# Performance work log

Measured on AMD Instinct MI355X. Metric: run time of the kernel, lower is better.

The kernel has to match this reference:

```python
import jax, jax.numpy as jnp
import numpy as np

E = 30000          # nEdges
K_PER_EDGE = 12    # quadruplets per edge
KMAX = 16          # padded K dimension
Q = E * K_PER_EDGE # nQuadruplets = 360000
I = 180000         # intermediate (db) expansion size
DE, DQ, DB = 128, 64, 64   # emb_size_edge, emb_size_quad, emb_size_bilinear
DRBF, DCBF, DSBF = 16, 16, 32
NSPH = 32
SCALE_SILU = 1.0 / 0.6


def _act(x):
    # GemNet ScaledSiLU
    return jax.nn.silu(x) * SCALE_SILU


def setup_inputs() -> dict:
    key = jax.random.key(0)
    ks = jax.random.split(key, 16)
    inp = {}
    inp["m"] = jax.random.normal(ks[0], (E, DE), jnp.float32)
    inp["rbf"] = jax.random.normal(ks[1], (E, DRBF), jnp.float32)
    inp["cbf"] = jax.random.normal(ks[2], (I, DCBF), jnp.float32)
    inp["sbf_W1"] = jax.random.normal(ks[3], (E, DSBF, NSPH), jnp.float32) * 0.1
    inp["sph"] = jax.random.normal(ks[4], (E, KMAX, NSPH), jnp.float32) * 0.1
    # structured, valid scatter indices: 12 distinct K-slots per edge
    inp["Kidx4"] = jnp.tile(jnp.arange(K_PER_EDGE, dtype=jnp.int32), E)
    inp["id4_reduce_ca"] = jnp.repeat(jnp.arange(E, dtype=jnp.int32), K_PER_EDGE)
    inp["id_swap"] = jax.random.permutation(ks[5], E).astype(jnp.int32)
    inp["id4_expand_intm_db"] = jax.random.randint(ks[6], (I,), 0, E, jnp.int32)
    inp["id4_expand_abd"] = jax.random.randint(ks[7], (Q,), 0, I, jnp.int32)
    # parameters (bias-free Dense layers + bilinear weight + scaling factors)
    def w(k, shape, fan_in):
        return jax.random.normal(k, shape, jnp.float32) / np.sqrt(fan_in)
    inp["W_db"] = w(ks[8], (DE, DE), DE)
    inp["W_rbf"] = w(ks[9], (DRBF, DE), DRBF)
    inp["W_down"] = w(ks[10], (DE, DQ), DE)
    inp["W_cbf"] = w(ks[11], (DCBF, DQ), DCBF)
    inp["W_bilin"] = w(ks[12], (DQ, DSBF, DB), DQ * DSBF)
    inp["W_up_ca"] = w(ks[13], (DB, DE), DB)
    inp["W_up_ac"] = w(ks[14], (DB, DE), DB)
    inp["s_rbf"] = jnp.asarray(1.1, jnp.float32)
    inp["s_cbf"] = jnp.asarray(0.9, jnp.float32)
    inp["s_sbf"] = jnp.asarray(1.2, jnp.float32)
    return inp


def reference(m, rbf, cbf, sbf_W1, sph,
              W_db, W_rbf, W_down, W_cbf, W_bilin, W_up_ca, W_up_ac,
              s_rbf, s_cbf, s_sbf,
              Kidx4, id_swap, id4_reduce_ca, id4_expand_intm_db, id4_expand_abd):
    # dense_db + hadamard with rbf MLP + scale
    x_db = _act(m @ W_db)                        # (E, DE)
    x_db = (x_db * (rbf @ W_rbf)) * s_rbf        # scale_rbf scales the product
    # down projection to quad size, expand to intermediate set
    x_db = _act(x_db @ W_down)                   # (E, DQ)
    x_db = x_db[id4_expand_intm_db]              # (I, DQ)
    # hadamard with cbf MLP + scale, expand to quadruplets
    x_db = (x_db * (cbf @ W_cbf)) * s_cbf        # (I, DQ)
    x_db = x_db[id4_expand_abd]                  # (Q, DQ)
    # EfficientInteractionBilinear: scatter quads into padded (E, Kmax, DQ)
    m2 = jnp.zeros((E, KMAX, DQ), x_db.dtype).at[id4_reduce_ca, Kidx4].set(x_db)
    sum_k = jnp.einsum("eks,ekq->esq", sph, m2)          # (E, NSPH, DQ)
    rw = jnp.einsum("eis,esq->eiq", sbf_W1, sum_k)       # (E, DSBF, DQ)
    x = jnp.einsum("eiq,qib->eb", rw, W_bilin)           # (E, DB)
    x = x * s_sbf                                         # scale_sbf_sum
    # up projections; swap directions for ac
    x_ca = _act(x @ W_up_ca)                     # (E, DE)
    x_ac = _act(x @ W_up_ac)[id_swap]            # (E, DE)
    return (x_ca + x_ac) * (1.0 / np.sqrt(2.0))
```

## Files before the change

kernel.cpp:

```cpp
#include <hip/hip_runtime.h>
#include <hip/hip_bf16.h>


#define E_N   30000
#define KPE   12
#define KMAXX 16
#define I_N   180000
#define DE    128
#define DQ    64
#define DB    64
#define DRBF  16
#define DCBF  16
#define DSBF  32
#define NSPH  32
#define SCALE_SILU (1.0f/0.6f)
#define INV_SQRT2  0.70710678118654752f

typedef __attribute__((ext_vector_type(8))) short bf16x8;
typedef __attribute__((ext_vector_type(4))) float f32x4;

__device__ __forceinline__ float silu_scaled(float x) {
    return x / (1.0f + __expf(-x)) * SCALE_SILU;
}

__device__ __forceinline__ short f2bf(float x) {
    unsigned u = __float_as_uint(x);
    u += 0x7fffu + ((u >> 16) & 1u);
    return (short)(u >> 16);
}

__device__ __forceinline__ bf16x8 cvt8(const float4 a, const float4 b) {
    bf16x8 t;
    t[0]=f2bf(a.x); t[1]=f2bf(a.y); t[2]=f2bf(a.z); t[3]=f2bf(a.w);
    t[4]=f2bf(b.x); t[5]=f2bf(b.y); t[6]=f2bf(b.z); t[7]=f2bf(b.w);
    return t;
}

#define PK_WDBT   0
#define PK_WRBFT  16384
#define PK_WDOWNT 20480
#define PK_WUPAT  28672
#define PK_WUPBT  36864
#define PK_BT     45056
#define PK_TOTAL  176128

__global__ __launch_bounds__(256) void kw_prep(
    const float* __restrict__ Wdb, const float* __restrict__ Wrbf,
    const float* __restrict__ Wdown, const float* __restrict__ WupA,
    const float* __restrict__ WupB, const float* __restrict__ Wbil,
    ushort* __restrict__ wpk)
{
    const int idx = blockIdx.x * 256 + threadIdx.x;
    float v;
    if (idx < PK_WRBFT) {
        const int n = idx >> 7, k = idx & 127;
        v = Wdb[k * DE + n];
    } else if (idx < PK_WDOWNT) {
        const int j = idx - PK_WRBFT;
        const int n = j >> 5, k = j & 31;
        v = (k < DRBF) ? Wrbf[k * DE + n] : 0.f;
    } else if (idx < PK_WUPAT) {
        const int j = idx - PK_WDOWNT;
        const int q = j >> 7, k = j & 127;
        v = Wdown[k * DQ + q];
    } else if (idx < PK_WUPBT) {
        const int j = idx - PK_WUPAT;
        const int d = j >> 6, b = j & 63;
        v = WupA[b * DE + d];
    } else if (idx < PK_BT) {
        const int j = idx - PK_WUPBT;
        const int d = j >> 6, b = j & 63;
        v = WupB[b * DE + d];
    } else {
        const int j = idx - PK_BT;
        const int b = j >> 11, jj = j & 2047;
        const int i = jj >> 6, q = jj & 63;
        v = Wbil[(size_t)(q * DSBF + i) * DB + b];
    }
    wpk[idx] = (ushort)f2bf(v);
}

__global__ __launch_bounds__(256) void k1_mfma(
    const float* __restrict__ m, const float* __restrict__ rbf,
    const ushort* __restrict__ wpk, const float* __restrict__ s_rbf_p,
    ushort* __restrict__ Tb)
{
    const int l  = threadIdx.x & 63;
    const int wv = __builtin_amdgcn_readfirstlane(threadIdx.x >> 6);
    const int e0 = (blockIdx.x * 4 + wv) * 16;
    if (e0 >= E_N) return;
    const int mr = l & 15;
    const int kg = l >> 4;
    const ushort* WdbT  = wpk + PK_WDBT;
    const ushort* WrbfT = wpk + PK_WRBFT;

    f32x4 accH[8], accR[8];
    #pragma unroll
    for (int nt = 0; nt < 8; ++nt)
        #pragma unroll
        for (int r = 0; r < 4; ++r) { accH[nt][r] = 0.f; accR[nt][r] = 0.f; }

    bf16x8 ra;
    if (kg < 2) {
        const float* rr = rbf + (size_t)(e0 + mr) * DRBF + kg * 8;
        ra = cvt8(*(const float4*)rr, *(const float4*)(rr + 4));
    } else {
        #pragma unroll
        for (int j = 0; j < 8; ++j) ra[j] = 0;
    }
    #pragma unroll
    for (int nt = 0; nt < 8; ++nt) {
        const bf16x8 rb = *(const bf16x8*)(WrbfT + (nt*16 + mr)*32 + kg*8);
        accR[nt] = __builtin_amdgcn_mfma_f32_16x16x32_bf16(ra, rb, accR[nt], 0,0,0);
    }

    const float* mrow = m + (size_t)(e0 + mr) * DE + kg * 8;
    #pragma unroll
    for (int kt = 0; kt < 4; ++kt) {
        const float* ms = mrow + kt * 32;
        const bf16x8 a = cvt8(*(const float4*)ms, *(const float4*)(ms + 4));
        #pragma unroll
        for (int nt = 0; nt < 8; ++nt) {
            const bf16x8 b = *(const bf16x8*)(WdbT + (nt*16 + mr)*128 + kt*32 + kg*8);
            accH[nt] = __builtin_amdgcn_mfma_f32_16x16x32_bf16(a, b, accH[nt], 0,0,0);
        }
    }

    const float srbf = s_rbf_p[0];
    ushort* tout = Tb + (size_t)(e0 + kg*4) * DE + mr;
    #pragma unroll
    for (int nt = 0; nt < 8; ++nt)
        #pragma unroll
        for (int r = 0; r < 4; ++r)
            tout[(size_t)r * DE + 16*nt] =
                (ushort)f2bf(silu_scaled(accH[nt][r]) * accR[nt][r] * srbf);
}

__global__ __launch_bounds__(256) void k1b_mfma(
    const ushort* __restrict__ Tb, const ushort* __restrict__ wpk,
    float* __restrict__ xq)
{
    const int l  = threadIdx.x & 63;
    const int wv = __builtin_amdgcn_readfirstlane(threadIdx.x >> 6);
    const int e0 = (blockIdx.x * 4 + wv) * 16;
    if (e0 >= E_N) return;
    const int mr = l & 15;
    const int kg = l >> 4;
    const ushort* WdownT = wpk + PK_WDOWNT;

    f32x4 acc[4];
    #pragma unroll
    for (int nt = 0; nt < 4; ++nt)
        #pragma unroll
        for (int r = 0; r < 4; ++r) acc[nt][r] = 0.f;

    const ushort* arow = Tb + (size_t)(e0 + mr) * DE + kg * 8;
    #pragma unroll
    for (int kt = 0; kt < 4; ++kt) {
        const bf16x8 a = *(const bf16x8*)(arow + kt * 32);
        #pragma unroll
        for (int nt = 0; nt < 4; ++nt) {
            const bf16x8 b = *(const bf16x8*)(WdownT + (nt*16 + mr)*128 + kt*32 + kg*8);
            acc[nt] = __builtin_amdgcn_mfma_f32_16x16x32_bf16(a, b, acc[nt], 0,0,0);
        }
    }
    float* xout = xq + (size_t)(e0 + kg*4) * DQ + mr;
    #pragma unroll
    for (int nt = 0; nt < 4; ++nt)
        #pragma unroll
        for (int r = 0; r < 4; ++r)
            xout[(size_t)r * DQ + 16*nt] = silu_scaled(acc[nt][r]);
}

__global__ __launch_bounds__(256) void k2_intm(
    const float* __restrict__ cbf, const int* __restrict__ idx_db,
    const float* __restrict__ xq, const float* __restrict__ Wcbf,
    const float* __restrict__ s_cbf_p, float* __restrict__ y)
{
    __shared__ float sW[DCBF*DQ];
    for (int i = threadIdx.x; i < DCBF*DQ; i += 256) sW[i] = Wcbf[i];
    __syncthreads();
    const float sc = s_cbf_p[0];
    const int lane = threadIdx.x & 63;
    const int wv = __builtin_amdgcn_readfirstlane(threadIdx.x >> 6);
    for (int row = blockIdx.x*4 + wv; row < I_N; row += gridDim.x*4) {
        const float* cr = cbf + (size_t)row*DCBF;
        float acc = 0.f;
        #pragma unroll
        for (int k = 0; k < DCBF; ++k) acc += cr[k] * sW[k*DQ + lane];
        const int src = idx_db[row];
        y[(size_t)row*DQ + lane] = xq[(size_t)src*DQ + lane] * acc * sc;
    }
}

__global__ __launch_bounds__(256) void k3a_rw(
    const float* __restrict__ y, const float* __restrict__ sph,
    const float* __restrict__ sbf, const int* __restrict__ kidx,
    const int* __restrict__ abd, ushort* __restrict__ rw)
{
    const int l  = threadIdx.x & 63;
    const int wv = __builtin_amdgcn_readfirstlane(threadIdx.x >> 6);
    const int e  = blockIdx.x*4 + wv;
    const int q0 = l & 15;
    const int sg = l >> 4;
    const int s0 = sg * 8;

    float SK[8][4];
    #pragma unroll
    for (int r = 0; r < 8; ++r)
        #pragma unroll
        for (int c = 0; c < 4; ++c) SK[r][c] = 0.f;

    const int base = e * KPE;
    #pragma unroll
    for (int j = 0; j < KPE; ++j) {
        const int kj = kidx[base + j];
        const int aj = abd[base + j];
        const float* yr = y + (size_t)aj * DQ;
        const float v0 = yr[q0];
        const float v1 = yr[q0 + 16];
        const float v2 = yr[q0 + 32];
        const float v3 = yr[q0 + 48];
        const float* sp = sph + ((size_t)e * KMAXX + kj) * NSPH + s0;
        const float4 sA = *(const float4*)sp;
        const float4 sB = *(const float4*)(sp + 4);
        const float sv[8] = {sA.x, sA.y, sA.z, sA.w, sB.x, sB.y, sB.z, sB.w};
        #pragma unroll
        for (int r = 0; r < 8; ++r) {
            SK[r][0] = __builtin_fmaf(sv[r], v0, SK[r][0]);
            SK[r][1] = __builtin_fmaf(sv[r], v1, SK[r][1]);
            SK[r][2] = __builtin_fmaf(sv[r], v2, SK[r][2]);
            SK[r][3] = __builtin_fmaf(sv[r], v3, SK[r][3]);
        }
    }

    bf16x8 bfrag[4];
    #pragma unroll
    for (int qt = 0; qt < 4; ++qt) {
        bf16x8 t;
        #pragma unroll
        for (int r = 0; r < 8; ++r) t[r] = f2bf(SK[r][qt]);
        bfrag[qt] = t;
    }

    const float* sb0 = sbf + ((size_t)e * DSBF + q0) * NSPH + s0;
    bf16x8 afrag[2];
    #pragma unroll
    for (int h = 0; h < 2; ++h) {
        const float* ar = sb0 + h * 16 * NSPH;
        afrag[h] = cvt8(*(const float4*)ar, *(const float4*)(ar + 4));
    }

    f32x4 acc[2][4];
    #pragma unroll
    for (int h = 0; h < 2; ++h)
        #pragma unroll
        for (int qt = 0; qt < 4; ++qt)
            #pragma unroll
            for (int r = 0; r < 4; ++r) acc[h][qt][r] = 0.f;

    #pragma unroll
    for (int h = 0; h < 2; ++h)
        #pragma unroll
        for (int qt = 0; qt < 4; ++qt)
            acc[h][qt] = __builtin_amdgcn_mfma_f32_16x16x32_bf16(
                afrag[h], bfrag[qt], acc[h][qt], 0, 0, 0);

    ushort* ro = rw + (size_t)e * (DSBF * DQ);
    #pragma unroll
    for (int h = 0; h < 2; ++h)
        #pragma unroll
        for (int r = 0; r < 4; ++r) {
            const int i = h * 16 + sg * 4 + r;
            #pragma unroll
            for (int qt = 0; qt < 4; ++qt)
                ro[i * DQ + q0 + 16 * qt] = (ushort)f2bf(acc[h][qt][r]);
        }
}

__global__ __launch_bounds__(256) void k3b_bilin(
    const ushort* __restrict__ rw, const ushort* __restrict__ wpk,
    const float* __restrict__ s_sbf_p, ushort* __restrict__ Xb)
{
    const int l  = threadIdx.x & 63;
    const int wv = __builtin_amdgcn_readfirstlane(threadIdx.x >> 6);
    const int e0 = (blockIdx.x * 4 + wv) * 16;
    if (e0 >= E_N) return;
    const int m  = l & 15;
    const int kg = l >> 4;
    const ushort* BT = wpk + PK_BT;

    const ushort* arow = rw + (size_t)(e0 + m) * 2048 + kg * 8;
    const ushort* b0   = BT + (size_t)m * 2048 + kg * 8;

    f32x4 acc[4];
    #pragma unroll
    for (int qt = 0; qt < 4; ++qt)
        #pragma unroll
        for (int r = 0; r < 4; ++r) acc[qt][r] = 0.f;

    #pragma unroll 4
    for (int kt = 0; kt < 64; ++kt) {
        const bf16x8 a = *(const bf16x8*)(arow + kt * 32);
        #pragma unroll
        for (int qt = 0; qt < 4; ++qt) {
            const bf16x8 b = *(const bf16x8*)(b0 + (size_t)qt * 16 * 2048 + kt * 32);
            acc[qt] = __builtin_amdgcn_mfma_f32_16x16x32_bf16(a, b, acc[qt], 0, 0, 0);
        }
    }

    const float ss = s_sbf_p[0];
    ushort* xout = Xb + (size_t)(e0 + kg*4) * DQ + m;
    #pragma unroll
    for (int qt = 0; qt < 4; ++qt)
        #pragma unroll
        for (int r = 0; r < 4; ++r)
            xout[(size_t)r * DQ + 16*qt] = (ushort)f2bf(acc[qt][r] * ss);
}

__global__ __launch_bounds__(256) void k4_mfma(
    const ushort* __restrict__ Xb, const ushort* __restrict__ wpk,
    float* __restrict__ Ab, float* __restrict__ Bb)
{
    const int l  = threadIdx.x & 63;
    const int wv = __builtin_amdgcn_readfirstlane(threadIdx.x >> 6);
    const int e0 = (blockIdx.x * 4 + wv) * 16;
    if (e0 >= E_N) return;
    const int mr = l & 15;
    const int kg = l >> 4;
    const ushort* WupAT = wpk + PK_WUPAT;
    const ushort* WupBT = wpk + PK_WUPBT;

    f32x4 accA[8], accB[8];
    #pragma unroll
    for (int nt = 0; nt < 8; ++nt)
        #pragma unroll
        for (int r = 0; r < 4; ++r) { accA[nt][r] = 0.f; accB[nt][r] = 0.f; }

    const ushort* arow = Xb + (size_t)(e0 + mr) * DQ + kg * 8;
    #pragma unroll
    for (int kt = 0; kt < 2; ++kt) {
        const bf16x8 a = *(const bf16x8*)(arow + kt * 32);
        #pragma unroll
        for (int nt = 0; nt < 8; ++nt) {
            const bf16x8 bA = *(const bf16x8*)(WupAT + (nt*16 + mr)*64 + kt*32 + kg*8);
            accA[nt] = __builtin_amdgcn_mfma_f32_16x16x32_bf16(a, bA, accA[nt], 0,0,0);
            const bf16x8 bB = *(const bf16x8*)(WupBT + (nt*16 + mr)*64 + kt*32 + kg*8);
            accB[nt] = __builtin_amdgcn_mfma_f32_16x16x32_bf16(a, bB, accB[nt], 0,0,0);
        }
    }
    float* aout = Ab + (size_t)(e0 + kg*4) * DE + mr;
    float* bout = Bb + (size_t)(e0 + kg*4) * DE + mr;
    #pragma unroll
    for (int nt = 0; nt < 8; ++nt)
        #pragma unroll
        for (int r = 0; r < 4; ++r) {
            aout[(size_t)r * DE + 16*nt] = silu_scaled(accA[nt][r]);
            bout[(size_t)r * DE + 16*nt] = silu_scaled(accB[nt][r]);
        }
}

__global__ __launch_bounds__(256) void k5_comb(
    const float* __restrict__ Ab, const float* __restrict__ Bb,
    const int* __restrict__ swp, float* __restrict__ out)
{
    const int i4   = blockIdx.x*256 + threadIdx.x;
    const int flat = i4*4;
    const int e = flat >> 7;
    const int d = flat & 127;
    const float4 a = *(const float4*)(Ab + flat);
    const int es = swp[e];
    const float4 b = *(const float4*)(Bb + (size_t)es*DE + d);
    float4 o = make_float4((a.x+b.x)*INV_SQRT2, (a.y+b.y)*INV_SQRT2,
                           (a.z+b.z)*INV_SQRT2, (a.w+b.w)*INV_SQRT2);
    *(float4*)(out + flat) = o;
}

extern "C" void kernel_launch(void* const* d_in, const int* in_sizes, int n_in,
                              void* d_out, int out_size, void* d_ws, size_t ws_size,
                              hipStream_t stream)
{
    const float* m      = (const float*)d_in[0];
    const float* rbf    = (const float*)d_in[1];
    const float* cbf    = (const float*)d_in[2];
    const float* sbfW1  = (const float*)d_in[3];
    const float* sph    = (const float*)d_in[4];
    const int*   kidx   = (const int*)d_in[5];
    const int*   idswap = (const int*)d_in[7];
    const int*   idin   = (const int*)d_in[8];
    const int*   abd    = (const int*)d_in[9];
    const float* Wdb    = (const float*)d_in[10];
    const float* Wrbf   = (const float*)d_in[11];
    const float* Wdown  = (const float*)d_in[12];
    const float* Wcbf   = (const float*)d_in[13];
    const float* Wbil   = (const float*)d_in[14];
    const float* WupA   = (const float*)d_in[15];
    const float* WupB   = (const float*)d_in[16];
    const float* s_rbf  = (const float*)d_in[17];
    const float* s_cbf  = (const float*)d_in[18];
    const float* s_sbf  = (const float*)d_in[19];
    float* out = (float*)d_out;

    float* ws  = (float*)d_ws;
    ushort* Tb = (ushort*)ws;
    float* xq  = ws +  1920000;
    float* y   = ws +  3840000;
    ushort* Xb = (ushort*)(ws + 15360000);
    float* Ab  = ws + 16320000;
    float* Bb  = ws + 20160000;
    ushort* rw = (ushort*)(ws + 24000000);
    ushort* wpk= (ushort*)(ws + 54720000);

    kw_prep  <<<688,  256, 0, stream>>>(Wdb, Wrbf, Wdown, WupA, WupB, Wbil, wpk);
    k1_mfma  <<<469,  256, 0, stream>>>(m, rbf, wpk, s_rbf, Tb);
    k1b_mfma <<<469,  256, 0, stream>>>(Tb, wpk, xq);
    k2_intm  <<<1024, 256, 0, stream>>>(cbf, idin, xq, Wcbf, s_cbf, y);
    k3a_rw   <<<7500, 256, 0, stream>>>(y, sph, sbfW1, kidx, abd, rw);
    k3b_bilin<<<469,  256, 0, stream>>>(rw, wpk, s_sbf, Xb);
    k4_mfma  <<<469,  256, 0, stream>>>(Xb, wpk, Ab, Bb);
    k5_comb  <<<3750, 256, 0, stream>>>(Ab, Bb, idswap, out);
}
```

Measured before the change: 498.2 us.

## Fuse rw computation and bilinear GEMM through swizzled shared memory

Merges the per-edge rw kernel and the bilinear contraction into one kernel. Each block computes rw for 16 edges into 64KB of XOR-swizzled LDS, then each wave runs the 2048-deep bilinear MFMA for one 16-column output slice. This removes the bf16 rw round trip through global memory (about 123MB written and read back). The cost is 64KB of LDS per block, which limits occupancy, and a serial four-edge loop per wave before a block-wide barrier.

```diff
diff --git a/kernel.cpp b/kernel.cpp
--- a/kernel.cpp
+++ b/kernel.cpp
@@ -193,129 +193,122 @@
     }
 }
 
-__global__ __launch_bounds__(256) void k3a_rw(
+__global__ __launch_bounds__(256) void k3_fused(
     const float* __restrict__ y, const float* __restrict__ sph,
     const float* __restrict__ sbf, const int* __restrict__ kidx,
-    const int* __restrict__ abd, ushort* __restrict__ rw)
-{
+    const int* __restrict__ abd, const ushort* __restrict__ wpk,
+    const float* __restrict__ s_sbf_p, ushort* __restrict__ Xb)
+{
+    __shared__ ushort sRw[16 * 2048];
     const int l  = threadIdx.x & 63;
     const int wv = __builtin_amdgcn_readfirstlane(threadIdx.x >> 6);
-    const int e  = blockIdx.x*4 + wv;
+    const int e0 = blockIdx.x * 16;
     const int q0 = l & 15;
     const int sg = l >> 4;
     const int s0 = sg * 8;
 
-    float SK[8][4];
-    #pragma unroll
-    for (int r = 0; r < 8; ++r)
-        #pragma unroll
-        for (int c = 0; c < 4; ++c) SK[r][c] = 0.f;
-
-    const int base = e * KPE;
-    #pragma unroll
-    for (int j = 0; j < KPE; ++j) {
-        const int kj = kidx[base + j];
-        const int aj = abd[base + j];
-        const float* yr = y + (size_t)aj * DQ;
-        const float v0 = yr[q0];
-        const float v1 = yr[q0 + 16];
-        const float v2 = yr[q0 + 32];
-        const float v3 = yr[q0 + 48];
-        const float* sp = sph + ((size_t)e * KMAXX + kj) * NSPH + s0;
-        const float4 sA = *(const float4*)sp;
-        const float4 sB = *(const float4*)(sp + 4);
-        const float sv[8] = {sA.x, sA.y, sA.z, sA.w, sB.x, sB.y, sB.z, sB.w};
-        #pragma unroll
-        for (int r = 0; r < 8; ++r) {
-            SK[r][0] = __builtin_fmaf(sv[r], v0, SK[r][0]);
-            SK[r][1] = __builtin_fmaf(sv[r], v1, SK[r][1]);
-            SK[r][2] = __builtin_fmaf(sv[r], v2, SK[r][2]);
-            SK[r][3] = __builtin_fmaf(sv[r], v3, SK[r][3]);
-        }
-    }
-
-    bf16x8 bfrag[4];
-    #pragma unroll
-    for (int qt = 0; qt < 4; ++qt) {
-        bf16x8 t;
-        #pragma unroll
-        for (int r = 0; r < 8; ++r) t[r] = f2bf(SK[r][qt]);
-        bfrag[qt] = t;
-    }
-
-    const float* sb0 = sbf + ((size_t)e * DSBF + q0) * NSPH + s0;
-    bf16x8 afrag[2];
-    #pragma unroll
-    for (int h = 0; h < 2; ++h) {
-        const float* ar = sb0 + h * 16 * NSPH;
-        afrag[h] = cvt8(*(const float4*)ar, *(const float4*)(ar + 4));
-    }
-
-    f32x4 acc[2][4];
-    #pragma unroll
-    for (int h = 0; h < 2; ++h)
-        #pragma unroll
-        for (int qt = 0; qt < 4; ++qt)
-            #pragma unroll
-            for (int r = 0; r < 4; ++r) acc[h][qt][r] = 0.f;
-
-    #pragma unroll
-    for (int h = 0; h < 2; ++h)
-        #pragma unroll
-        for (int qt = 0; qt < 4; ++qt)
-            acc[h][qt] = __builtin_amdgcn_mfma_f32_16x16x32_bf16(
-                afrag[h], bfrag[qt], acc[h][qt], 0, 0, 0);
-
-    ushort* ro = rw + (size_t)e * (DSBF * DQ);
-    #pragma unroll
-    for (int h = 0; h < 2; ++h)
-        #pragma unroll
-        for (int r = 0; r < 4; ++r) {
-            const int i = h * 16 + sg * 4 + r;
+    for (int ei = 0; ei < 4; ++ei) {
+        const int eL = wv * 4 + ei;
+        const int e  = e0 + eL;
+
+        float SK[8][4];
+        #pragma unroll
+        for (int r = 0; r < 8; ++r)
+            #pragma unroll
+            for (int c = 0; c < 4; ++c) SK[r][c] = 0.f;
+
+        const int base = e * KPE;
+        #pragma unroll
+        for (int j = 0; j < KPE; ++j) {
+            const int kj = kidx[base + j];
+            const int aj = abd[base + j];
+            const float* yr = y + (size_t)aj * DQ;
+            const float v0 = yr[q0];
+            const float v1 = yr[q0 + 16];
+            const float v2 = yr[q0 + 32];
+            const float v3 = yr[q0 + 48];
+            const float* sp = sph + ((size_t)e * KMAXX + kj) * NSPH + s0;
+            const float4 sA = *(const float4*)sp;
+            const float4 sB = *(const float4*)(sp + 4);
+            const float sv[8] = {sA.x, sA.y, sA.z, sA.w, sB.x, sB.y, sB.z, sB.w};
+            #pragma unroll
+            for (int r = 0; r < 8; ++r) {
+                SK[r][0] = __builtin_fmaf(sv[r], v0, SK[r][0]);
+                SK[r][1] = __builtin_fmaf(sv[r], v1, SK[r][1]);
+                SK[r][2] = __builtin_fmaf(sv[r], v2, SK[r][2]);
+                SK[r][3] = __builtin_fmaf(sv[r], v3, SK[r][3]);
+            }
+        }
+
+        bf16x8 bfrag[4];
+        #pragma unroll
+        for (int qt = 0; qt < 4; ++qt) {
+            bf16x8 t;
+            #pragma unroll
+            for (int r = 0; r < 8; ++r) t[r] = f2bf(SK[r][qt]);
+            bfrag[qt] = t;
+        }
+
+        const float* sb0 = sbf + ((size_t)e * DSBF + q0) * NSPH + s0;
+        bf16x8 afrag[2];
+        #pragma unroll
+        for (int h = 0; h < 2; ++h) {
+            const float* ar = sb0 + h * 16 * NSPH;
+            afrag[h] = cvt8(*(const float4*)ar, *(const float4*)(ar + 4));
+        }
+
+        f32x4 acc[2][4];
+        #pragma unroll
+        for (int h = 0; h < 2; ++h)
             #pragma unroll
             for (int qt = 0; qt < 4; ++qt)
-                ro[i * DQ + q0 + 16 * qt] = (ushort)f2bf(acc[h][qt][r]);
-        }
-}
-
-__global__ __launch_bounds__(256) void k3b_bilin(
-    const ushort* __restrict__ rw, const ushort* __restrict__ wpk,
-    const float* __restrict__ s_sbf_p, ushort* __restrict__ Xb)
-{
-    const int l  = threadIdx.x & 63;
-    const int wv = __builtin_amdgcn_readfirstlane(threadIdx.x >> 6);
-    const int e0 = (blockIdx.x * 4 + wv) * 16;
-    if (e0 >= E_N) return;
-    const int m  = l & 15;
-    const int kg = l >> 4;
-    const ushort* BT = wpk + PK_BT;
-
-    const ushort* arow = rw + (size_t)(e0 + m) * 2048 + kg * 8;
-    const ushort* b0   = BT + (size_t)m * 2048 + kg * 8;
-
-    f32x4 acc[4];
-    #pragma unroll
-    for (int qt = 0; qt < 4; ++qt)
-        #pragma unroll
-        for (int r = 0; r < 4; ++r) acc[qt][r] = 0.f;
-
-    #pragma unroll 4
+                #pragma unroll
+                for (int r = 0; r < 4; ++r) acc[h][qt][r] = 0.f;
+
+        #pragma unroll
+        for (int h = 0; h < 2; ++h)
+            #pragma unroll
+            for (int qt = 0; qt < 4; ++qt)
+                acc[h][qt] = __builtin_amdgcn_mfma_f32_16x16x32_bf16(
+                    afrag[h], bfrag[qt], acc[h][qt], 0, 0, 0);
+
+        ushort* ro = sRw + eL * 2048;
+        const int swz = (eL & 7) << 3;
+        #pragma unroll
+        for (int h = 0; h < 2; ++h)
+            #pragma unroll
+            for (int r = 0; r < 4; ++r) {
+                const int i = h * 16 + sg * 4 + r;
+                #pragma unroll
+                for (int qt = 0; qt < 4; ++qt)
+                    ro[(i * DQ + q0 + 16 * qt) ^ swz] =
+                        (ushort)f2bf(acc[h][qt][r]);
+            }
+    }
+    __syncthreads();
+
+    const int eA  = l & 15;
+    const int kg  = l >> 4;
+    const int swzA = (eA & 7) << 3;
+    const ushort* brow = wpk + PK_BT + (size_t)(wv * 16 + (l & 15)) * 2048 + kg * 8;
+
+    f32x4 xacc;
+    #pragma unroll
+    for (int r = 0; r < 4; ++r) xacc[r] = 0.f;
+
+    #pragma unroll 8
     for (int kt = 0; kt < 64; ++kt) {
-        const bf16x8 a = *(const bf16x8*)(arow + kt * 32);
-        #pragma unroll
-        for (int qt = 0; qt < 4; ++qt) {
-            const bf16x8 b = *(const bf16x8*)(b0 + (size_t)qt * 16 * 2048 + kt * 32);
-            acc[qt] = __builtin_amdgcn_mfma_f32_16x16x32_bf16(a, b, acc[qt], 0, 0, 0);
-        }
+        const bf16x8 a = *(const bf16x8*)(sRw + eA * 2048 +
+                                          ((kt * 32 + kg * 8) ^ swzA));
+        const bf16x8 b = *(const bf16x8*)(brow + kt * 32);
+        xacc = __builtin_amdgcn_mfma_f32_16x16x32_bf16(a, b, xacc, 0, 0, 0);
     }
 
     const float ss = s_sbf_p[0];
-    ushort* xout = Xb + (size_t)(e0 + kg*4) * DQ + m;
-    #pragma unroll
-    for (int qt = 0; qt < 4; ++qt)
-        #pragma unroll
-        for (int r = 0; r < 4; ++r)
-            xout[(size_t)r * DQ + 16*qt] = (ushort)f2bf(acc[qt][r] * ss);
+    ushort* xout = Xb + (size_t)(e0 + kg * 4) * DQ + wv * 16 + (l & 15);
+    #pragma unroll
+    for (int r = 0; r < 4; ++r)
+        xout[(size_t)r * DQ] = (ushort)f2bf(xacc[r] * ss);
 }
 
 __global__ __launch_bounds__(256) void k4_mfma(
@@ -408,15 +401,13 @@
     ushort* Xb = (ushort*)(ws + 15360000);
     float* Ab  = ws + 16320000;
     float* Bb  = ws + 20160000;
-    ushort* rw = (ushort*)(ws + 24000000);
-    ushort* wpk= (ushort*)(ws + 54720000);
+    ushort* wpk= (ushort*)(ws + 24000000);
 
     kw_prep  <<<688,  256, 0, stream>>>(Wdb, Wrbf, Wdown, WupA, WupB, Wbil, wpk);
     k1_mfma  <<<469,  256, 0, stream>>>(m, rbf, wpk, s_rbf, Tb);
     k1b_mfma <<<469,  256, 0, stream>>>(Tb, wpk, xq);
     k2_intm  <<<1024, 256, 0, stream>>>(cbf, idin, xq, Wcbf, s_cbf, y);
-    k3a_rw   <<<7500, 256, 0, stream>>>(y, sph, sbfW1, kidx, abd, rw);
-    k3b_bilin<<<469,  256, 0, stream>>>(rw, wpk, s_sbf, Xb);
+    k3_fused <<<1875, 256, 0, stream>>>(y, sph, sbfW1, kidx, abd, wpk, s_sbf, Xb);
     k4_mfma  <<<469,  256, 0, stream>>>(Xb, wpk, Ab, Bb);
     k5_comb  <<<3750, 256, 0, stream>>>(Ab, Bb, idswap, out);
 }
```

Result: faster. 472.6 us (-5.1%).
